# Kernel tuning notes

Hardware: AMD Instinct MI355X
Metric: run time of the kernel (lower is better)

Reference implementation:

```python
import jax, jax.numpy as jnp
import numpy as np

E = 64          # num_routed_experts
K = 6           # num_experts_per_token
NS = 2          # num_shared_experts
D = 512         # hidden_size
F = 512         # expert_intermediate_size = intermediate_size // 4


def setup_inputs() -> dict:
    key = jax.random.key(0)
    ks = jax.random.split(key, 8)
    s = 0.02
    return {
        "hidden_states": jax.random.normal(ks[0], (2, 1024, D), dtype=jnp.float32),
        "Wr": jax.random.normal(ks[1], (D, E), dtype=jnp.float32) * s,      # router
        "sWg": jax.random.normal(ks[2], (NS, D, F), dtype=jnp.float32) * s,  # shared gate_proj
        "sWu": jax.random.normal(ks[3], (NS, D, F), dtype=jnp.float32) * s,  # shared up_proj
        "sWd": jax.random.normal(ks[4], (NS, F, D), dtype=jnp.float32) * s,  # shared down_proj
        "Wg": jax.random.normal(ks[5], (E, D, F), dtype=jnp.float32) * s,    # routed gate_proj
        "Wu": jax.random.normal(ks[6], (E, D, F), dtype=jnp.float32) * s,    # routed up_proj
        "Wd": jax.random.normal(ks[7], (E, F, D), dtype=jnp.float32) * s,    # routed down_proj
    }


def _swiglu_ffn(x, wg, wu, wd):
    # x: (N, D); wg/wu: (D, F); wd: (F, D)
    return (jax.nn.silu(x @ wg) * (x @ wu)) @ wd


def reference(hidden_states, Wr, sWg, sWu, sWd, Wg, Wu, Wd):
    B, S, d = hidden_states.shape
    x = hidden_states.reshape(-1, d)  # (N, D)
    N = x.shape[0]

    # ---- shared experts (always on) ----
    shared = jnp.zeros_like(x)
    for e in range(NS):
        shared = shared + _swiglu_ffn(x, sWg[e], sWu[e], sWd[e])

    # ---- top-k router ----
    logits = x @ Wr                                   # (N, E)
    probs = jax.nn.softmax(logits, axis=-1)
    top_w, top_i = jax.lax.top_k(probs, K)            # (N, K)
    top_w = top_w / jnp.sum(top_w, axis=-1, keepdims=True)  # renormalize
    gate = jnp.zeros((N, E), dtype=x.dtype).at[jnp.arange(N)[:, None], top_i].set(top_w)

    # ---- routed experts: per-expert FFN, combined with sparse gate ----
    routed = jnp.zeros_like(x)
    for e in range(E):
        routed = routed + _swiglu_ffn(x, Wg[e], Wu[e], Wd[e]) * gate[:, e:e + 1]

    out = (shared + routed + x).reshape(B, S, d)
    return out
```

## Files before the change

kernel.cpp:

```cpp
#include <hip/hip_runtime.h>

#define N_TOK 2048
#define DD 512
#define FF 512
#define EE 64
#define TK 6
#define NG 66
#define RSLOT 12288
#define NSLOT 16384
#define BM 64
#define BN 64
#define BK 64
#define NKT 8
#define MAXT 320
#define MATSZ 262144

typedef float f32x4 __attribute__((ext_vector_type(4)));
typedef __bf16 bf16x8 __attribute__((ext_vector_type(8)));

__device__ __forceinline__ unsigned cvtpk(float lo, float hi) {
  unsigned r;
  asm("v_cvt_pk_bf16_f32 %0, %1, %2" : "=v"(r) : "v"(lo), "v"(hi));
  return r;
}

__device__ __forceinline__ void gll16(const void* g, void* l) {
  __builtin_amdgcn_global_load_lds(
      (const __attribute__((address_space(1))) unsigned int*)g,
      (__attribute__((address_space(3))) unsigned int*)l, 16, 0, 0);
}

__global__ __launch_bounds__(256) void convw_k(
    const float* __restrict__ Wg, const float* __restrict__ Wu, const float* __restrict__ Wd,
    const float* __restrict__ sWg, const float* __restrict__ sWu, const float* __restrict__ sWd,
    short* __restrict__ Wt) {
  int y = blockIdx.y;
  int kind = y / 66, idx = y % 66;
  const float* src;
  if (kind == 0)      src = (idx < EE) ? Wg + (size_t)idx * MATSZ : sWg + (size_t)(idx - EE) * MATSZ;
  else if (kind == 1) src = (idx < EE) ? Wu + (size_t)idx * MATSZ : sWu + (size_t)(idx - EE) * MATSZ;
  else                src = (idx < EE) ? Wd + (size_t)idx * MATSZ : sWd + (size_t)(idx - EE) * MATSZ;
  short* dst = Wt + (size_t)y * MATSZ;
  int f0 = blockIdx.x * 64;
  int lane = threadIdx.x & 63, w = threadIdx.x >> 6;
  int fl = lane & 15, dg = lane >> 4;
  const float* sp = src + (size_t)(dg * 8) * 512 + f0 + fl * 4;
  short* dp = dst + (size_t)(f0 + fl * 4) * 512 + dg * 8;
  f32x4 v[4][8];
#pragma unroll
  for (int it = 0; it < 4; ++it) {
    int db = (it * 4 + w) * 32;
#pragma unroll
    for (int jd = 0; jd < 8; ++jd)
      v[it][jd] = *(const f32x4*)(sp + (size_t)(db + jd) * 512);
  }
#pragma unroll
  for (int it = 0; it < 4; ++it) {
    int db = (it * 4 + w) * 32;
#pragma unroll
    for (int jf = 0; jf < 4; ++jf) {
      uint4 o;
      o.x = cvtpk(v[it][0][jf], v[it][1][jf]);
      o.y = cvtpk(v[it][2][jf], v[it][3][jf]);
      o.z = cvtpk(v[it][4][jf], v[it][5][jf]);
      o.w = cvtpk(v[it][6][jf], v[it][7][jf]);
      *(uint4*)(dp + (size_t)jf * 512 + db) = o;
    }
  }
}

__global__ void convx_k(const float* __restrict__ x, short* __restrict__ Xb) {
  int i = blockIdx.x * 256 + threadIdx.x;
  const f32x4* p = (const f32x4*)(x + (size_t)i * 8);
  f32x4 v0 = p[0], v1 = p[1];
  uint4 o;
  o.x = cvtpk(v0[0], v0[1]); o.y = cvtpk(v0[2], v0[3]);
  o.z = cvtpk(v1[0], v1[1]); o.w = cvtpk(v1[2], v1[3]);
  *(uint4*)&Xb[(size_t)i * 8] = o;
}

__global__ __launch_bounds__(256) void router_k(
    const float* __restrict__ x, const float* __restrict__ Wr,
    int* __restrict__ top_i, float* __restrict__ top_w, int* __restrict__ cnt) {
  __shared__ float xs[16 * 512];
  __shared__ float part[4][16][64];
  int tid = threadIdx.x, lane = tid & 63, w = tid >> 6;
  int t0 = blockIdx.x * 16;
  const f32x4* xin = (const f32x4*)(x + (size_t)t0 * DD);
  f32x4* xs4 = (f32x4*)xs;
#pragma unroll
  for (int i = 0; i < 8; ++i) xs4[i * 256 + tid] = xin[i * 256 + tid];
  __syncthreads();
  float acc[16];
#pragma unroll
  for (int t = 0; t < 16; ++t) acc[t] = 0.f;
  for (int kk = 0; kk < 32; ++kk) {
    int k = w * 128 + kk * 4;
    float w0 = Wr[(size_t)(k + 0) * EE + lane];
    float w1 = Wr[(size_t)(k + 1) * EE + lane];
    float w2 = Wr[(size_t)(k + 2) * EE + lane];
    float w3 = Wr[(size_t)(k + 3) * EE + lane];
#pragma unroll
    for (int t = 0; t < 16; ++t) {
      f32x4 xv = *(const f32x4*)&xs[t * 512 + k];
      acc[t] = fmaf(xv[0], w0, acc[t]);
      acc[t] = fmaf(xv[1], w1, acc[t]);
      acc[t] = fmaf(xv[2], w2, acc[t]);
      acc[t] = fmaf(xv[3], w3, acc[t]);
    }
  }
#pragma unroll
  for (int t = 0; t < 16; ++t) part[w][t][lane] = acc[t];
  __syncthreads();
#pragma unroll
  for (int tt = 0; tt < 4; ++tt) {
    int t = w * 4 + tt;
    float l0 = part[0][t][lane] + part[1][t][lane] + part[2][t][lane] + part[3][t][lane];
    float m = l0;
#pragma unroll
    for (int s = 32; s; s >>= 1) m = fmaxf(m, __shfl_xor(m, s));
    float p = __expf(l0 - m);
    int wi[TK]; float wv[TK];
#pragma unroll
    for (int it = 0; it < TK; ++it) {
      float v = p;
#pragma unroll
      for (int s = 32; s; s >>= 1) v = fmaxf(v, __shfl_xor(v, s));
      unsigned long long b = __ballot(p == v);
      int idx = __ffsll((unsigned long long)b) - 1;
      wi[it] = idx; wv[it] = v;
      if (lane == idx) p = -1.f;
    }
    float wsum = 0.f;
#pragma unroll
    for (int it = 0; it < TK; ++it) wsum += wv[it];
    int tg = t0 + t;
    if (lane < TK) {
      int si = 0; float sv = 0.f;
#pragma unroll
      for (int it = 0; it < TK; ++it) if (lane == it) { si = wi[it]; sv = wv[it]; }
      top_i[tg * TK + lane] = si;
      top_w[tg * TK + lane] = sv / wsum;
      atomicAdd(&cnt[si], 1);
    }
  }
}

__global__ void offsets_k(const int* __restrict__ cnt, int* __restrict__ goff,
                          int* __restrict__ fill, int* __restrict__ wk_g,
                          int* __restrict__ wk_mt, int* __restrict__ nitems) {
  int i = threadIdx.x;
  fill[i] = 0;
  int c = cnt[i];
  int s = c;
#pragma unroll
  for (int d = 1; d < 64; d <<= 1) { int t = __shfl_up(s, d); if (i >= d) s += t; }
  goff[i] = s - c;
  if (i == 63) {
    goff[EE] = RSLOT;
    goff[EE + 1] = RSLOT + N_TOK;
    goff[EE + 2] = RSLOT + 2 * N_TOK;
  }
  int nt = (c + BM - 1) >> 6;
  int ts = nt;
#pragma unroll
  for (int d = 1; d < 64; d <<= 1) { int t = __shfl_up(ts, d); if (i >= d) ts += t; }
  int texcl = ts - nt;
  for (int t = 0; t < nt; ++t) { wk_g[texcl + t] = i; wk_mt[texcl + t] = t; }
  int tot = __shfl(ts, 63);
  wk_g[tot + i] = EE + (i >> 5);
  wk_mt[tot + i] = i & 31;
  if (i == 0) nitems[0] = tot + 64;
}

__global__ void scatter_k(const int* __restrict__ top_i, const float* __restrict__ top_w,
                          const int* __restrict__ goff, int* __restrict__ fill,
                          int* __restrict__ btok, float* __restrict__ bw,
                          int* __restrict__ tslot) {
  int idx = blockIdx.x * blockDim.x + threadIdx.x;
  if (idx < RSLOT) {
    int e = top_i[idx];
    int pos = goff[e] + atomicAdd(&fill[e], 1);
    btok[pos] = idx / TK;
    bw[pos] = top_w[idx];
    tslot[idx] = pos;
  } else if (idx < NSLOT) {
    int j = idx - RSLOT;
    btok[idx] = j & (N_TOK - 1);
    bw[idx] = 1.0f;
  }
}

__global__ __launch_bounds__(256) void gemm1_k(
    const short* __restrict__ Xb, const short* __restrict__ Wtg, const short* __restrict__ Wtu,
    const int* __restrict__ goff, const int* __restrict__ btok,
    const int* __restrict__ wk_g, const int* __restrict__ wk_mt,
    const int* __restrict__ nitems, short* __restrict__ H) {
  int item = blockIdx.y;
  if (item >= nitems[0]) return;
  int g = wk_g[item], mt = wk_mt[item];
  int s0g = goff[g], cnt = goff[g + 1] - s0g;
  int n0 = blockIdx.x * BN;
  const short* gmat = Wtg + (size_t)g * MATSZ;
  const short* umat = Wtu + (size_t)g * MATSZ;

  __shared__ __align__(16) short lds[2][12288];

  int tid = threadIdx.x, lane = tid & 63, w = tid >> 6;
  int wr = w >> 1, wc = w & 1;
  int lr = lane & 15, lgq = lane >> 4;
  int s0 = s0g + mt * BM;

  const short* sp[6];
  int ldst[6];
#pragma unroll
  for (int q = 0; q < 6; ++q) {
    int c = w * 6 + q;
    ldst[q] = c * 512;
    int rl = (c & 7) * 8 + (lane >> 3);
    int u = (lane & 7) ^ (rl & 7);
    if (c < 8) {
      int slot = (mt * BM + rl < cnt) ? s0 + rl : s0;
      sp[q] = Xb + (size_t)btok[slot] * 512 + u * 8;
    } else if (c < 16) {
      sp[q] = gmat + (size_t)(n0 + rl) * 512 + u * 8;
    } else {
      sp[q] = umat + (size_t)(n0 + rl) * 512 + u * 8;
    }
  }

  f32x4 accg[2][2], accu[2][2];
#pragma unroll
  for (int i = 0; i < 2; ++i)
#pragma unroll
    for (int j = 0; j < 2; ++j) {
      accg[i][j] = f32x4{0.f, 0.f, 0.f, 0.f};
      accu[i][j] = f32x4{0.f, 0.f, 0.f, 0.f};
    }

  auto STAGE = [&](int b, int kt) {
#pragma unroll
    for (int q = 0; q < 6; ++q) gll16(sp[q] + kt * 64, &lds[b][ldst[q]]);
  };
  auto COMPUTE = [&](int b) {
    const short* L = lds[b];
#pragma unroll
    for (int ks = 0; ks < 2; ++ks) {
      bf16x8 af[2], bg[2], bu[2];
#pragma unroll
      for (int i = 0; i < 2; ++i) {
        int row = wr * 32 + i * 16 + lr;
        af[i] = *(const bf16x8*)&L[row * 64 + (((ks * 4 + lgq) ^ (row & 7)) * 8)];
      }
#pragma unroll
      for (int j = 0; j < 2; ++j) {
        int fr = wc * 32 + j * 16 + lr;
        int o = fr * 64 + (((ks * 4 + lgq) ^ (fr & 7)) * 8);
        bg[j] = *(const bf16x8*)&L[4096 + o];
        bu[j] = *(const bf16x8*)&L[8192 + o];
      }
#pragma unroll
      for (int i = 0; i < 2; ++i)
#pragma unroll
        for (int j = 0; j < 2; ++j) {
          accg[i][j] = __builtin_amdgcn_mfma_f32_16x16x32_bf16(af[i], bg[j], accg[i][j], 0, 0, 0);
          accu[i][j] = __builtin_amdgcn_mfma_f32_16x16x32_bf16(af[i], bu[j], accu[i][j], 0, 0, 0);
        }
    }
  };

  STAGE(0, 0);
  __syncthreads();
  int b = 0;
#pragma unroll 1
  for (int kt = 0; kt < NKT; ++kt) {
    if (kt + 1 < NKT) STAGE(b ^ 1, kt + 1);
    COMPUTE(b);
    __syncthreads();
    b ^= 1;
  }

#pragma unroll
  for (int i = 0; i < 2; ++i)
#pragma unroll
    for (int j = 0; j < 2; ++j)
#pragma unroll
      for (int r = 0; r < 4; ++r) {
        int mrow = wr * 32 + i * 16 + lgq * 4 + r;
        if (mt * BM + mrow < cnt) {
          float gg = accg[i][j][r];
          float uu = accu[i][j][r];
          float hv = (gg / (1.f + __expf(-gg))) * uu;
          int col = n0 + wc * 32 + j * 16 + lr;
          H[(size_t)(s0 + mrow) * FF + col] = (short)(cvtpk(hv, hv) & 0xffffu);
        }
      }
}

__global__ __launch_bounds__(256) void gemm2_k(
    const short* __restrict__ H, const short* __restrict__ Wtd,
    const int* __restrict__ goff, const float* __restrict__ bw,
    const int* __restrict__ wk_g, const int* __restrict__ wk_mt,
    const int* __restrict__ nitems, short* __restrict__ Osl) {
  int item = blockIdx.y;
  if (item >= nitems[0]) return;
  int g = wk_g[item], mt = wk_mt[item];
  int s0g = goff[g], cnt = goff[g + 1] - s0g;
  int n0 = blockIdx.x * BN;
  const short* dmat = Wtd + (size_t)g * MATSZ;

  __shared__ __align__(16) short lds[2][8192];

  int tid = threadIdx.x, lane = tid & 63, w = tid >> 6;
  int wr = w >> 1, wc = w & 1;
  int lr = lane & 15, lgq = lane >> 4;
  int s0 = s0g + mt * BM;

  const short* sp[4];
  int ldst[4];
#pragma unroll
  for (int q = 0; q < 4; ++q) {
    int c = w * 4 + q;
    ldst[q] = c * 512;
    int rl = (c & 7) * 8 + (lane >> 3);
    int u = (lane & 7) ^ (rl & 7);
    if (c < 8) {
      int slot = (mt * BM + rl < cnt) ? s0 + rl : s0;
      sp[q] = H + (size_t)slot * 512 + u * 8;
    } else {
      sp[q] = dmat + (size_t)(n0 + rl) * 512 + u * 8;
    }
  }

  f32x4 acc[2][2];
#pragma unroll
  for (int i = 0; i < 2; ++i)
#pragma unroll
    for (int j = 0; j < 2; ++j) acc[i][j] = f32x4{0.f, 0.f, 0.f, 0.f};

  auto STAGE = [&](int b, int kt) {
#pragma unroll
    for (int q = 0; q < 4; ++q) gll16(sp[q] + kt * 64, &lds[b][ldst[q]]);
  };
  auto COMPUTE = [&](int b) {
    const short* L = lds[b];
#pragma unroll
    for (int ks = 0; ks < 2; ++ks) {
      bf16x8 af[2], bd[2];
#pragma unroll
      for (int i = 0; i < 2; ++i) {
        int row = wr * 32 + i * 16 + lr;
        af[i] = *(const bf16x8*)&L[row * 64 + (((ks * 4 + lgq) ^ (row & 7)) * 8)];
      }
#pragma unroll
      for (int j = 0; j < 2; ++j) {
        int dr = wc * 32 + j * 16 + lr;
        bd[j] = *(const bf16x8*)&L[4096 + dr * 64 + (((ks * 4 + lgq) ^ (dr & 7)) * 8)];
      }
#pragma unroll
      for (int i = 0; i < 2; ++i)
#pragma unroll
        for (int j = 0; j < 2; ++j)
          acc[i][j] = __builtin_amdgcn_mfma_f32_16x16x32_bf16(af[i], bd[j], acc[i][j], 0, 0, 0);
    }
  };

  STAGE(0, 0);
  __syncthreads();
  int b = 0;
#pragma unroll 1
  for (int kt = 0; kt < NKT; ++kt) {
    if (kt + 1 < NKT) STAGE(b ^ 1, kt + 1);
    COMPUTE(b);
    __syncthreads();
    b ^= 1;
  }

#pragma unroll
  for (int i = 0; i < 2; ++i)
#pragma unroll
    for (int r = 0; r < 4; ++r) {
      int mrow = wr * 32 + i * 16 + lgq * 4 + r;
      if (mt * BM + mrow < cnt) {
        int slot = s0 + mrow;
        float wv = bw[slot];
#pragma unroll
        for (int j = 0; j < 2; ++j) {
          int col = n0 + wc * 32 + j * 16 + lr;
          Osl[(size_t)slot * DD + col] = (short)(cvtpk(acc[i][j][r] * wv, 0.f) & 0xffffu);
        }
      }
    }
}

__global__ __launch_bounds__(256) void combine_k(
    const short* __restrict__ Osl, const float* __restrict__ x,
    const int* __restrict__ tslot, float* __restrict__ out) {
  int wv = threadIdx.x >> 6, lane = threadIdx.x & 63;
  int t = blockIdx.x * 4 + wv;
  int d0 = lane * 8;
  const float* xp = x + (size_t)t * DD + d0;
  f32x4 sa = *(const f32x4*)xp;
  f32x4 sb = *(const f32x4*)(xp + 4);
  int slots[8];
#pragma unroll
  for (int k = 0; k < 6; ++k) slots[k] = tslot[t * TK + k];
  slots[6] = RSLOT + t;
  slots[7] = RSLOT + N_TOK + t;
#pragma unroll
  for (int k = 0; k < 8; ++k) {
    uint4 hv = *(const uint4*)&Osl[(size_t)slots[k] * DD + d0];
    unsigned u[4] = {hv.x, hv.y, hv.z, hv.w};
#pragma unroll
    for (int q = 0; q < 4; ++q) {
      float lo = __builtin_bit_cast(float, u[q] << 16);
      float hi = __builtin_bit_cast(float, u[q] & 0xffff0000u);
      if (q < 2) { sa[q * 2] += lo; sa[q * 2 + 1] += hi; }
      else { sb[(q - 2) * 2] += lo; sb[(q - 2) * 2 + 1] += hi; }
    }
  }
  float* op = out + (size_t)t * DD + d0;
  *(f32x4*)op = sa;
  *(f32x4*)(op + 4) = sb;
}

extern "C" void kernel_launch(void* const* d_in, const int* in_sizes, int n_in,
                              void* d_out, int out_size, void* d_ws, size_t ws_size,
                              hipStream_t stream) {
  const float* x   = (const float*)d_in[0];
  const float* Wr  = (const float*)d_in[1];
  const float* sWg = (const float*)d_in[2];
  const float* sWu = (const float*)d_in[3];
  const float* sWd = (const float*)d_in[4];
  const float* Wg  = (const float*)d_in[5];
  const float* Wu  = (const float*)d_in[6];
  const float* Wd  = (const float*)d_in[7];
  float* out = (float*)d_out;

  char* wsb = (char*)d_ws;
  size_t off = 0;
  short* Wt = (short*)(wsb + off);    off += (size_t)198 * MATSZ * 2;
  short* H  = (short*)(wsb + off);    off += (size_t)NSLOT * FF * 2;
  short* Osl = (short*)(wsb + off);   off += (size_t)NSLOT * DD * 2;
  short* Xb = (short*)(wsb + off);    off += (size_t)N_TOK * DD * 2;
  int*   top_i = (int*)(wsb + off);   off += (size_t)RSLOT * 4;
  float* top_w = (float*)(wsb + off); off += (size_t)RSLOT * 4;
  int*   btok = (int*)(wsb + off);    off += (size_t)NSLOT * 4;
  float* bwt  = (float*)(wsb + off);  off += (size_t)NSLOT * 4;
  int*   tslot = (int*)(wsb + off);   off += (size_t)RSLOT * 4;
  int*   cnt  = (int*)(wsb + off);    off += 256;
  int*   fill = (int*)(wsb + off);    off += 256;
  int*   goff = (int*)(wsb + off);    off += 512;
  int*   wk_g = (int*)(wsb + off);    off += MAXT * 4;
  int*   wk_mt = (int*)(wsb + off);   off += MAXT * 4;
  int*   nitems = (int*)(wsb + off);  off += 256;

  const short* Wtg = Wt;
  const short* Wtu = Wt + (size_t)66 * MATSZ;
  const short* Wtd = Wt + (size_t)132 * MATSZ;

  hipMemsetAsync(cnt, 0, 256, stream);
  convw_k<<<dim3(8, 198), 256, 0, stream>>>(Wg, Wu, Wd, sWg, sWu, sWd, Wt);
  convx_k<<<512, 256, 0, stream>>>(x, Xb);
  router_k<<<N_TOK / 16, 256, 0, stream>>>(x, Wr, top_i, top_w, cnt);
  offsets_k<<<1, 64, 0, stream>>>(cnt, goff, fill, wk_g, wk_mt, nitems);
  scatter_k<<<NSLOT / 256, 256, 0, stream>>>(top_i, top_w, goff, fill, btok, bwt, tslot);
  dim3 grid1(FF / BN, MAXT, 1);
  gemm1_k<<<grid1, 256, 0, stream>>>(Xb, Wtg, Wtu, goff, btok, wk_g, wk_mt, nitems, H);
  dim3 grid2(DD / BN, MAXT, 1);
  gemm2_k<<<grid2, 256, 0, stream>>>(H, Wtd, goff, bwt, wk_g, wk_mt, nitems, Osl);
  combine_k<<<N_TOK / 4, 256, 0, stream>>>(Osl, x, tslot, out);
}
```

Measured before the change: 224.8 us.

## Transpose weights through padded LDS tiles in fp32-to-bf16 conversion kernel

Rewrites the weight conversion/transpose kernel to stage 64x32 fp32 tiles in padded shared memory, so both the global reads and the bf16 writes are coalesced. The grid grows from 8 to 128 blocks per matrix, giving much more parallelism and less register pressure per thread. This targets the memory-bound weight conversion pass, which moves about 200MB per call. The cost is an LDS round trip and a barrier per tile.

```diff
diff --git a/kernel.cpp b/kernel.cpp
--- a/kernel.cpp
+++ b/kernel.cpp
@@ -34,6 +34,7 @@
     const float* __restrict__ Wg, const float* __restrict__ Wu, const float* __restrict__ Wd,
     const float* __restrict__ sWg, const float* __restrict__ sWu, const float* __restrict__ sWd,
     short* __restrict__ Wt) {
+  __shared__ float T[64][33];
   int y = blockIdx.y;
   int kind = y / 66, idx = y % 66;
   const float* src;
@@ -41,32 +42,24 @@
   else if (kind == 1) src = (idx < EE) ? Wu + (size_t)idx * MATSZ : sWu + (size_t)(idx - EE) * MATSZ;
   else                src = (idx < EE) ? Wd + (size_t)idx * MATSZ : sWd + (size_t)(idx - EE) * MATSZ;
   short* dst = Wt + (size_t)y * MATSZ;
-  int f0 = blockIdx.x * 64;
-  int lane = threadIdx.x & 63, w = threadIdx.x >> 6;
-  int fl = lane & 15, dg = lane >> 4;
-  const float* sp = src + (size_t)(dg * 8) * 512 + f0 + fl * 4;
-  short* dp = dst + (size_t)(f0 + fl * 4) * 512 + dg * 8;
-  f32x4 v[4][8];
-#pragma unroll
-  for (int it = 0; it < 4; ++it) {
-    int db = (it * 4 + w) * 32;
-#pragma unroll
-    for (int jd = 0; jd < 8; ++jd)
-      v[it][jd] = *(const f32x4*)(sp + (size_t)(db + jd) * 512);
-  }
-#pragma unroll
-  for (int it = 0; it < 4; ++it) {
-    int db = (it * 4 + w) * 32;
-#pragma unroll
-    for (int jf = 0; jf < 4; ++jf) {
-      uint4 o;
-      o.x = cvtpk(v[it][0][jf], v[it][1][jf]);
-      o.y = cvtpk(v[it][2][jf], v[it][3][jf]);
-      o.z = cvtpk(v[it][4][jf], v[it][5][jf]);
-      o.w = cvtpk(v[it][6][jf], v[it][7][jf]);
-      *(uint4*)(dp + (size_t)jf * 512 + db) = o;
-    }
-  }
+  int d0 = (blockIdx.x & 7) * 64;
+  int f0 = (blockIdx.x >> 3) * 32;
+  int t = threadIdx.x;
+
+  int r = t >> 3, fo = (t & 7) * 4;
+  const float* sp = src + (size_t)(d0 + r) * 512 + f0 + fo;
+  *(f32x4*)&T[r][fo]      = *(const f32x4*)sp;
+  *(f32x4*)&T[r + 32][fo] = *(const f32x4*)(sp + (size_t)32 * 512);
+  __syncthreads();
+
+  int f = t >> 3, a = t & 7, dd = a * 8;
+  float v[8];
+#pragma unroll
+  for (int i = 0; i < 8; ++i) v[i] = T[dd + i][f];
+  uint4 o;
+  o.x = cvtpk(v[0], v[1]); o.y = cvtpk(v[2], v[3]);
+  o.z = cvtpk(v[4], v[5]); o.w = cvtpk(v[6], v[7]);
+  *(uint4*)&dst[(size_t)(f0 + f) * 512 + d0 + dd] = o;
 }
 
 __global__ void convx_k(const float* __restrict__ x, short* __restrict__ Xb) {
@@ -460,7 +453,7 @@
   const short* Wtd = Wt + (size_t)132 * MATSZ;
 
   hipMemsetAsync(cnt, 0, 256, stream);
-  convw_k<<<dim3(8, 198), 256, 0, stream>>>(Wg, Wu, Wd, sWg, sWu, sWd, Wt);
+  convw_k<<<dim3(128, 198), 256, 0, stream>>>(Wg, Wu, Wd, sWg, sWu, sWd, Wt);
   convx_k<<<512, 256, 0, stream>>>(x, Xb);
   router_k<<<N_TOK / 16, 256, 0, stream>>>(x, Wr, top_i, top_w, cnt);
   offsets_k<<<1, 64, 0, stream>>>(cnt, goff, fill, wk_g, wk_mt, nitems);
```

Result: faster. 214.8 us (-4.4%).
